# Optimization experiments

Measured on AMD Instinct MI355X. Metric: run time of the kernel, lower is better.

Reference implementation:

```python
import jax, jax.numpy as jnp
import numpy as np

B, D, L = 4096, 128, 4
ALPHA = 1.0
SLOPE = 0.1  # LeakyReLU negative slope


def _leaky(h):
    return jnp.where(h > 0, h, SLOPE * h)


def _dleaky(h):
    return jnp.where(h > 0, 1.0, SLOPE).astype(h.dtype)


def setup_inputs() -> dict:
    key = jax.random.key(0)
    ks = jax.random.split(key, 7)
    scale = 0.5 / np.sqrt(D)  # keep residual roughly Lipschitz < 1
    x = jax.random.normal(ks[0], (B, D), jnp.float32)
    W1 = jax.random.normal(ks[1], (L, D, D), jnp.float32) * scale
    b1 = jax.random.normal(ks[2], (L, D), jnp.float32) * 0.01
    W2 = jax.random.normal(ks[3], (L, D, D), jnp.float32) * scale
    b2 = jax.random.normal(ks[4], (L, D), jnp.float32) * 0.01
    W3 = jax.random.normal(ks[5], (L, D, D), jnp.float32) * scale
    b3 = jax.random.normal(ks[6], (L, D), jnp.float32) * 0.01
    return {"x": x, "W1": W1, "b1": b1, "W2": W2, "b2": b2, "W3": W3, "b3": b3}


def reference(x, W1, b1, W2, b2, W3, b3):
    logdet = jnp.zeros(x.shape[0], x.dtype)
    for i in range(L):  # small fixed number of structurally distinct blocks
        w1, w2, w3 = W1[i], W2[i], W3[i]
        # --- block forward: x <- x + alpha * f(x) ---
        h1 = x @ w1.T + b1[i]
        h2 = _leaky(h1) @ w2.T + b2[i]
        f = _leaky(h2) @ w3.T + b3[i]
        x = x + ALPHA * f
        # --- log|det J_f| evaluated at the NEW x (as in the original code) ---
        g1 = x @ w1.T + b1[i]          # [B, D] pre-activation 1
        d1 = _dleaky(g1)
        g2 = _leaky(g1) @ w2.T + b2[i]  # [B, D] pre-activation 2
        d2 = _dleaky(g2)
        # J[b] = w3 @ diag(d2[b]) @ w2 @ diag(d1[b]) @ w1  -> [B, D, D]
        J = (w3[None, :, :] * d2[:, None, :]) @ w2
        J = (J * d1[:, None, :]) @ w1
        s = jnp.linalg.svd(J, compute_uv=False)  # [B, D] singular values
        logdet = logdet + jnp.sum(jnp.log(s), axis=-1)
    return x, logdet
```

## Files before the change

kernel.cpp:

```cpp
#include <hip/hip_runtime.h>

typedef __attribute__((ext_vector_type(8))) short short8;
typedef __attribute__((ext_vector_type(4))) float float4f;
typedef __attribute__((ext_vector_type(4))) unsigned short us4;

#define PITCH 136
#define ROWS 32
#define LOG_SLOPE -2.302585092994046f
#define LN2 0.6931471805599453f
#define NBLK 140
#define LDS_BYTES 69760
#define WS_BIAS 4160
#define WS_WPLANES 8192
#define NWELEM 196608

__device__ __forceinline__ float bf2f(unsigned int u) {
    return __builtin_bit_cast(float, u << 16);
}
__device__ __forceinline__ unsigned short f2bf(float f) {
    unsigned int x = __builtin_bit_cast(unsigned int, f);
    x += 0x7fff + ((x >> 16) & 1);
    return (unsigned short)(x >> 16);
}
__device__ __forceinline__ float4f vmsub(float4f a, float s, float4f b) {
    a[0] -= s * b[0]; a[1] -= s * b[1]; a[2] -= s * b[2]; a[3] -= s * b[3];
    return a;
}
__device__ __forceinline__ float4f vscale(float4f a, float s) {
    a[0] *= s; a[1] *= s; a[2] *= s; a[3] *= s;
    return a;
}

__device__ __forceinline__ void bar_lgkm() {
    asm volatile("s_waitcnt lgkmcnt(0)\n\ts_barrier" ::: "memory");
}

template<int ISF32>
__device__ __forceinline__ float ldv(const void* p, int i) {
    if (ISF32) return ((const float*)p)[i];
    return bf2f(((const unsigned short*)p)[i]);
}

__device__ __forceinline__ int detect_f32(const unsigned short* W1u, int lane) {
    unsigned int u = W1u[lane * 2];
    unsigned int e = (u >> 7) & 0xFF;
    int bad = (e < 64) || (e > 135);
    return __ballot(bad) != 0ull;
}

__device__ __forceinline__ float4f mfma16(short8 a, short8 b, float4f c) {
    return __builtin_amdgcn_mfma_f32_16x16x32_bf16(a, b, c, 0, 0, 0);
}

__device__ __forceinline__ void split8(float4f a, float4f b, short8& hi, short8& lo) {
#pragma unroll
    for (int j = 0; j < 4; ++j) {
        float v = a[j]; unsigned short h = f2bf(v);
        hi[j] = (short)h; lo[j] = (short)f2bf(v - bf2f(h));
        v = b[j]; h = f2bf(v);
        hi[4 + j] = (short)h; lo[4 + j] = (short)f2bf(v - bf2f(h));
    }
}

__global__ void k_prep(const void* __restrict__ W1, const void* __restrict__ W2,
                       const void* __restrict__ W3, const void* __restrict__ b1,
                       const void* __restrict__ b2, const void* __restrict__ b3,
                       float* __restrict__ ws) {
    const int tid = threadIdx.x, bid = blockIdx.x;
    const int isf32 = detect_f32((const unsigned short*)W1, tid & 63);
    unsigned short* whi = (unsigned short*)(ws + WS_WPLANES);
    unsigned short* wlo = whi + NWELEM;
    if (bid < 96) {
        int s = (bid * 256 + tid) * 8;
        int mat = s >> 14, off = s & 16383;
        int wsel = mat >> 2;
        const void* Wm = wsel == 0 ? W1 : (wsel == 1 ? W2 : W3);
        int src = (mat & 3) * 16384 + off;
        short8 hi, lo;
        if (isf32) {
            const float* p = (const float*)Wm + src;
            split8(*(const float4f*)p, *(const float4f*)(p + 4), hi, lo);
        } else {
            hi = *(const short8*)((const unsigned short*)Wm + src);
            lo = (short8){0, 0, 0, 0, 0, 0, 0, 0};
        }
        int c = off >> 7, k = off & 127;
        int kk = k >> 5, q = (k >> 3) & 3;
        int cb = c >> 4, m = c & 15;
        int noff = kk * 4096 + cb * 512 + m * 32 + q * 8;
        *(short8*)(whi + mat * 16384 + noff) = hi;
        *(short8*)(wlo + mat * 16384 + noff) = lo;
    } else {
        for (int e = tid; e < 1536; e += 256) {
            int bsel = e >> 9, idx = e & 511;
            const void* bp = bsel == 0 ? b1 : (bsel == 1 ? b2 : b3);
            ws[WS_BIAS + e] = isf32 ? ((const float*)bp)[idx]
                                    : bf2f(((const unsigned short*)bp)[idx]);
        }
        if (tid == 0) ((int*)ws)[0] = 0;
    }
}

template<int ISF32> struct WT { short8 v[ISF32 ? 16 : 8]; };

template<int ISF32>
__device__ __forceinline__ WT<ISF32> loadW(const unsigned short* __restrict__ wh,
                                           const unsigned short* __restrict__ wl,
                                           int cb, int mq) {
    WT<ISF32> r;
#pragma unroll
    for (int kk = 0; kk < 4; ++kk) {
        const int o0 = kk * 4096 + cb * 512 + mq;
        const int o1 = o0 + 512;
        if (ISF32) {
            r.v[kk * 4 + 0] = *(const short8*)(wh + o0);
            r.v[kk * 4 + 1] = *(const short8*)(wh + o1);
            r.v[kk * 4 + 2] = *(const short8*)(wl + o0);
            r.v[kk * 4 + 3] = *(const short8*)(wl + o1);
        } else {
            r.v[kk * 2 + 0] = *(const short8*)(wh + o0);
            r.v[kk * 2 + 1] = *(const short8*)(wh + o1);
        }
    }
    return r;
}

template<int MODE, int DOLOAD, int ISF32>
__device__ __forceinline__ WT<ISF32> matvec(const WT<ISF32>& w,
        const unsigned short* inh, const unsigned short* inl,
        unsigned short* outh, unsigned short* outl,
        const unsigned short* resh, const unsigned short* resl,
        const unsigned short* __restrict__ nwh, const unsigned short* __restrict__ nwl,
        const float* __restrict__ bias,
        int lane, int colb, int* cnt) {
    const int m = lane & 15, q = lane >> 4;
    float4f b0 = *(const float4f*)(bias + colb + q * 4);
    float4f b1 = *(const float4f*)(bias + colb + 16 + q * 4);
    float4f acc[2][2];
    acc[0][0] = b0; acc[0][1] = b1;
    acc[1][0] = b0; acc[1][1] = b1;
    bar_lgkm();
    WT<ISF32> wn;
    if constexpr (DOLOAD) {
        wn = loadW<ISF32>(nwh, nwl, colb >> 4, m * 32 + q * 8);
    }
#pragma unroll
    for (int kk = 0; kk < 4; ++kk) {
        const int kc = kk * 32 + q * 8;
#pragma unroll
        for (int rt = 0; rt < 2; ++rt) {
            short8 xh = *(const short8*)(inh + (rt * 16 + m) * PITCH + kc);
            short8 xl = *(const short8*)(inl + (rt * 16 + m) * PITCH + kc);
            if (ISF32) {
                acc[rt][0] = mfma16(w.v[kk * 4 + 0], xh, acc[rt][0]);
                acc[rt][0] = mfma16(w.v[kk * 4 + 0], xl, acc[rt][0]);
                acc[rt][0] = mfma16(w.v[kk * 4 + 2], xh, acc[rt][0]);
                acc[rt][1] = mfma16(w.v[kk * 4 + 1], xh, acc[rt][1]);
                acc[rt][1] = mfma16(w.v[kk * 4 + 1], xl, acc[rt][1]);
                acc[rt][1] = mfma16(w.v[kk * 4 + 3], xh, acc[rt][1]);
            } else {
                acc[rt][0] = mfma16(w.v[kk * 2 + 0], xh, acc[rt][0]);
                acc[rt][0] = mfma16(w.v[kk * 2 + 0], xl, acc[rt][0]);
                acc[rt][1] = mfma16(w.v[kk * 2 + 1], xh, acc[rt][1]);
                acc[rt][1] = mfma16(w.v[kk * 2 + 1], xl, acc[rt][1]);
            }
        }
    }
    int cc[2] = {0, 0};
#pragma unroll
    for (int rt = 0; rt < 2; ++rt) {
#pragma unroll
        for (int ct = 0; ct < 2; ++ct) {
            float4f v = acc[rt][ct];
            const int o = (rt * 16 + m) * PITCH + colb + ct * 16 + q * 4;
            if (MODE == 1) {
                us4 rh = *(const us4*)(resh + o);
                us4 rl = *(const us4*)(resl + o);
#pragma unroll
                for (int j = 0; j < 4; ++j) v[j] += bf2f(rh[j]) + bf2f(rl[j]);
            }
            if (MODE >= 2) {
#pragma unroll
                for (int j = 0; j < 4; ++j) cc[rt] += (v[j] <= 0.0f) ? 1 : 0;
            }
            if (MODE == 0 || MODE == 2) {
#pragma unroll
                for (int j = 0; j < 4; ++j) v[j] = v[j] > 0.0f ? v[j] : 0.1f * v[j];
            }
            if (MODE != 3) {
                us4 h, l;
#pragma unroll
                for (int j = 0; j < 4; ++j) {
                    unsigned short hh = f2bf(v[j]);
                    h[j] = hh;
                    l[j] = f2bf(v[j] - bf2f(hh));
                }
                *(us4*)(outh + o) = h;
                *(us4*)(outl + o) = l;
            }
        }
    }
    if (MODE >= 2) {
#pragma unroll
        for (int rt = 0; rt < 2; ++rt) {
            int c = cc[rt];
            c += __shfl_xor(c, 16);
            c += __shfl_xor(c, 32);
            if (q == 0) atomicAdd(&cnt[rt * 16 + m], c);
        }
    }
    if constexpr (DOLOAD) return wn;
    else return w;
}

template<int ISF32>
__device__ __forceinline__ void fwd(int bid, int tid, int lane, char* ldsb,
                                    const void* x, const float* ws, void* out,
                                    float* wsw) {
    unsigned short* P = (unsigned short*)ldsb;
    unsigned short* Ah = P;
    unsigned short* Al = P + 1 * ROWS * PITCH;
    unsigned short* Bh = P + 2 * ROWS * PITCH;
    unsigned short* Bl = P + 3 * ROWS * PITCH;
    unsigned short* Th = P + 4 * ROWS * PITCH;
    unsigned short* Tl = P + 5 * ROWS * PITCH;
    unsigned short* Uh = P + 6 * ROWS * PITCH;
    unsigned short* Ul = P + 7 * ROWS * PITCH;
    int* cnt = (int*)(P + 8 * ROWS * PITCH);
    const unsigned short* whi = (const unsigned short*)(ws + WS_WPLANES);
    const unsigned short* wlo = whi + NWELEM;
    const float* bias = ws + WS_BIAS;
    const int r0 = bid * ROWS;
    const int m = lane & 15, q = lane >> 4;
    const int colb = (tid >> 6) * 32;
    WT<ISF32> wA = loadW<ISF32>(whi, wlo, colb >> 4, m * 32 + q * 8);
    WT<ISF32> wB, wC;
    for (int e = tid; e < ROWS * 128; e += 256) {
        int r = e >> 7, c = e & 127;
        float v = ldv<ISF32>(x, (r0 + r) * 128 + c);
        unsigned short h = f2bf(v);
        Ah[r * PITCH + c] = h;
        Al[r * PITCH + c] = f2bf(v - bf2f(h));
    }
    if (tid < ROWS) cnt[tid] = 0;
    unsigned short *curh = Ah, *curl = Al, *othh = Bh, *othl = Bl;
#pragma unroll 1
    for (int layer = 0; layer < 4; ++layer) {
        const unsigned short* w2h = whi + (4 + layer) * 16384;
        const unsigned short* w2l = wlo + (4 + layer) * 16384;
        const unsigned short* w3h = whi + (8 + layer) * 16384;
        const unsigned short* w3l = wlo + (8 + layer) * 16384;
        const unsigned short* n1h = whi + ((layer + 1) & 3) * 16384;
        const unsigned short* n1l = wlo + ((layer + 1) & 3) * 16384;
        const float* b1p = bias + layer * 128;
        const float* b2p = bias + 512 + layer * 128;
        const float* b3p = bias + 1024 + layer * 128;
        wB = matvec<0, 1, ISF32>(wA, curh, curl, Th, Tl, 0, 0, w2h, w2l, b1p, lane, colb, cnt);
        wC = matvec<0, 1, ISF32>(wB, Th, Tl, Uh, Ul, 0, 0, w3h, w3l, b2p, lane, colb, cnt);
        matvec<1, 0, ISF32>(wC, Uh, Ul, othh, othl, curh, curl, 0, 0, b3p, lane, colb, cnt);
        matvec<2, 0, ISF32>(wA, othh, othl, Th, Tl, 0, 0, 0, 0, b1p, lane, colb, cnt);
        wA = matvec<3, 1, ISF32>(wB, Th, Tl, Th, Tl, 0, 0, n1h, n1l, b2p, lane, colb, cnt);
        unsigned short* t;
        t = curh; curh = othh; othh = t;
        t = curl; curl = othl; othl = t;
    }
    bar_lgkm();
    for (int e = tid; e < ROWS * 128; e += 256) {
        int r = e >> 7, c = e & 127;
        float v = bf2f(curh[r * PITCH + c]) + bf2f(curl[r * PITCH + c]);
        if (ISF32) ((float*)out)[(r0 + r) * 128 + c] = v;
        else ((unsigned short*)out)[(r0 + r) * 128 + c] = f2bf(v);
    }
    if (tid < ROWS) wsw[64 + r0 + tid] = (float)cnt[tid];
}

template<int ISF32>
__device__ __forceinline__ float lu_logdet(int id, int tid, float* lds,
        const void* W1, const void* W2, const void* W3) {
    const int wsel = id % 3;
    const void* Wm = (wsel == 0 ? W1 : (wsel == 1 ? W2 : W3));
    const int ofs = (id / 3) * 16384;
    const int tx = tid & 31, ty = tid >> 5;
    float* rowbuf = lds;
    float* colbuf = lds + 1024;
    float4f V[16];
#pragma unroll
    for (int m = 0; m < 16; ++m) {
        int base = ofs + (ty + 8 * m) * 128 + 4 * tx;
        if (ISF32) {
            V[m] = *(const float4f*)((const float*)Wm + base);
        } else {
            ushort4 u = *(const ushort4*)((const unsigned short*)Wm + base);
            V[m] = (float4f){bf2f(u.x), bf2f(u.y), bf2f(u.z), bf2f(u.w)};
        }
    }
    if (ty < 4) *(float4f*)&rowbuf[ty * 128 + 4 * tx] = V[0];
    if (tx == 0) {
#pragma unroll
        for (int j = 0; j < 4; ++j) {
#pragma unroll
            for (int mg = 0; mg < 4; ++mg) {
                float4f t = {V[mg * 4 + 0][j], V[mg * 4 + 1][j],
                             V[mg * 4 + 2][j], V[mg * 4 + 3][j]};
                *(float4f*)&colbuf[j * 128 + ty * 16 + mg * 4] = t;
            }
        }
    }
    __syncthreads();
    float logacc = 0.0f;
#pragma unroll 1
    for (int kap = 0; kap < 32; ++kap) {
        const int K = kap * 4;
        const int buf = (kap & 1) * 512;
        float4f D[4], R[4], C[4][4];
#pragma unroll
        for (int j = 0; j < 4; ++j) {
            D[j] = *(const float4f*)&rowbuf[buf + j * 128 + K];
            R[j] = *(const float4f*)&rowbuf[buf + j * 128 + 4 * tx];
#pragma unroll
            for (int mg = 0; mg < 4; ++mg)
                C[j][mg] = *(const float4f*)&colbuf[buf + j * 128 + ty * 16 + mg * 4];
        }
        float p0 = D[0][0], i0 = 1.0f / p0;
        float l10 = D[1][0] * i0, l20 = D[2][0] * i0, l30 = D[3][0] * i0;
        D[1] = vmsub(D[1], l10, D[0]); R[1] = vmsub(R[1], l10, R[0]);
        D[2] = vmsub(D[2], l20, D[0]); R[2] = vmsub(R[2], l20, R[0]);
        D[3] = vmsub(D[3], l30, D[0]); R[3] = vmsub(R[3], l30, R[0]);
        float p1 = D[1][1], i1 = 1.0f / p1;
        float l21 = D[2][1] * i1, l31 = D[3][1] * i1;
        D[2] = vmsub(D[2], l21, D[1]); R[2] = vmsub(R[2], l21, R[1]);
        D[3] = vmsub(D[3], l31, D[1]); R[3] = vmsub(R[3], l31, R[1]);
        float p2 = D[2][2], i2 = 1.0f / p2;
        float l32 = D[3][2] * i2;
        D[3] = vmsub(D[3], l32, D[2]); R[3] = vmsub(R[3], l32, R[2]);
        float p3 = D[3][3], i3 = 1.0f / p3;
        logacc += __log2f(fabsf(p0)) + __log2f(fabsf(p1))
                + __log2f(fabsf(p2)) + __log2f(fabsf(p3));
        float4f X3 = vscale(R[3], i3);
        float4f X2 = vscale(vmsub(R[2], D[2][3], X3), i2);
        float4f X1 = vscale(vmsub(vmsub(R[1], D[1][2], X2), D[1][3], X3), i1);
        float4f X0 = vscale(vmsub(vmsub(vmsub(R[0], D[0][1], X1),
                                        D[0][2], X2), D[0][3], X3), i0);
#pragma unroll
        for (int mg = 0; mg < 4; ++mg) {
#pragma unroll
            for (int e = 0; e < 4; ++e) {
                float4f v = V[mg * 4 + e];
                v = vmsub(v, C[0][mg][e], X0);
                v = vmsub(v, C[1][mg][e], X1);
                v = vmsub(v, C[2][mg][e], X2);
                v = vmsub(v, C[3][mg][e], X3);
                V[mg * 4 + e] = v;
            }
        }
        if (kap < 31) {
            const int nbuf = ((kap + 1) & 1) * 512;
            const int tb = (kap & 1) ? 0 : 4;
            const int mn = (kap + 1) >> 1;
            if (ty >= tb && ty < tb + 4) {
                float4f val;
                switch (mn) {
                case 0:  val = V[0];  break; case 1:  val = V[1];  break;
                case 2:  val = V[2];  break; case 3:  val = V[3];  break;
                case 4:  val = V[4];  break; case 5:  val = V[5];  break;
                case 6:  val = V[6];  break; case 7:  val = V[7];  break;
                case 8:  val = V[8];  break; case 9:  val = V[9];  break;
                case 10: val = V[10]; break; case 11: val = V[11]; break;
                case 12: val = V[12]; break; case 13: val = V[13]; break;
                case 14: val = V[14]; break; default: val = V[15]; break;
                }
                *(float4f*)&rowbuf[nbuf + (ty - tb) * 128 + 4 * tx] = val;
            }
            if (tx == kap + 1) {
#pragma unroll
                for (int j = 0; j < 4; ++j) {
#pragma unroll
                    for (int mg = 0; mg < 4; ++mg) {
                        float4f t = {V[mg * 4 + 0][j], V[mg * 4 + 1][j],
                                     V[mg * 4 + 2][j], V[mg * 4 + 3][j]};
                        *(float4f*)&colbuf[nbuf + j * 128 + ty * 16 + mg * 4] = t;
                    }
                }
            }
        }
        __syncthreads();
    }
    return logacc * LN2;
}

__global__ __launch_bounds__(256, 1) void k_main(
        const void* __restrict__ x,
        const void* __restrict__ W1, const void* __restrict__ b1,
        const void* __restrict__ W2, const void* __restrict__ b2,
        const void* __restrict__ W3, const void* __restrict__ b3,
        void* __restrict__ out, float* __restrict__ ws) {
    extern __shared__ __align__(16) char ldsb[];
    __shared__ int s_last;
    const int tid = threadIdx.x;
    const int lane = tid & 63;
    const int isf32 = detect_f32((const unsigned short*)W1, lane);

    if (blockIdx.x < 12) {
        float ld = isf32 ? lu_logdet<1>(blockIdx.x, tid, (float*)ldsb, W1, W2, W3)
                         : lu_logdet<0>(blockIdx.x, tid, (float*)ldsb, W1, W2, W3);
        if (tid == 0) ws[2 + blockIdx.x] = ld;
    } else {
        const int bid = blockIdx.x - 12;
        if (isf32) fwd<1>(bid, tid, lane, ldsb, x, ws, out, ws);
        else       fwd<0>(bid, tid, lane, ldsb, x, ws, out, ws);
    }

    __threadfence();
    if (tid == 0) s_last = (atomicAdd((int*)ws, 1) == NBLK - 1);
    __syncthreads();
    if (!s_last) return;
    __threadfence();
    float s = 0.0f;
#pragma unroll
    for (int i = 0; i < 12; ++i) s += ws[2 + i];
    for (int b = tid; b < 4096; b += 256) {
        float v = s + LOG_SLOPE * ws[64 + b];
        if (isf32) ((float*)out)[524288 + b] = v;
        else ((unsigned short*)out)[524288 + b] = f2bf(v);
    }
}

extern "C" void kernel_launch(void* const* d_in, const int* in_sizes, int n_in,
                              void* d_out, int out_size, void* d_ws, size_t ws_size,
                              hipStream_t stream) {
    const void* x  = d_in[0];
    const void* W1 = d_in[1];
    const void* b1 = d_in[2];
    const void* W2 = d_in[3];
    const void* b2 = d_in[4];
    const void* W3 = d_in[5];
    const void* b3 = d_in[6];
    float* ws = (float*)d_ws;

    hipLaunchKernelGGL(k_prep, dim3(97), dim3(256), 0, stream,
                       W1, W2, W3, b1, b2, b3, ws);
    hipLaunchKernelGGL(k_main, dim3(NBLK), dim3(256), LDS_BYTES, stream,
                       x, W1, b1, W2, b2, W3, b3, d_out, ws);
}
```

Measured before the change: 119.4 us.

## Interleave two LU factorizations per block to share barriers and cut block count

Each LU-logdet block now factors two weight matrices at once, interleaving their elimination steps inside one loop so the two sets of independent work overlap and share one barrier per step. The block count falls from 12 LU blocks to 6, so the grid shrinks from 140 to 134. The intent is to hide the per-step LDS and barrier latency of the serial LU chain with independent work. The cost is doubled register state per thread (two sets of 16 float4 values), which risks spills, and twice the work per LU block on the critical path.

```diff
diff --git a/kernel.cpp b/kernel.cpp
--- a/kernel.cpp
+++ b/kernel.cpp
@@ -8,7 +8,7 @@
 #define ROWS 32
 #define LOG_SLOPE -2.302585092994046f
 #define LN2 0.6931471805599453f
-#define NBLK 140
+#define NBLK 134
 #define LDS_BYTES 69760
 #define WS_BIAS 4160
 #define WS_WPLANES 8192
@@ -275,117 +275,120 @@
 }
 
 template<int ISF32>
-__device__ __forceinline__ float lu_logdet(int id, int tid, float* lds,
-        const void* W1, const void* W2, const void* W3) {
+struct LUState { float4f V[16]; };
+
+template<int ISF32>
+__device__ __forceinline__ void lu_init(LUState<ISF32>& S, int id,
+        const void* W1, const void* W2, const void* W3, int tx, int ty) {
     const int wsel = id % 3;
     const void* Wm = (wsel == 0 ? W1 : (wsel == 1 ? W2 : W3));
     const int ofs = (id / 3) * 16384;
-    const int tx = tid & 31, ty = tid >> 5;
-    float* rowbuf = lds;
-    float* colbuf = lds + 1024;
-    float4f V[16];
 #pragma unroll
     for (int m = 0; m < 16; ++m) {
         int base = ofs + (ty + 8 * m) * 128 + 4 * tx;
         if (ISF32) {
-            V[m] = *(const float4f*)((const float*)Wm + base);
+            S.V[m] = *(const float4f*)((const float*)Wm + base);
         } else {
             ushort4 u = *(const ushort4*)((const unsigned short*)Wm + base);
-            V[m] = (float4f){bf2f(u.x), bf2f(u.y), bf2f(u.z), bf2f(u.w)};
-        }
-    }
-    if (ty < 4) *(float4f*)&rowbuf[ty * 128 + 4 * tx] = V[0];
+            S.V[m] = (float4f){bf2f(u.x), bf2f(u.y), bf2f(u.z), bf2f(u.w)};
+        }
+    }
+}
+
+template<int ISF32>
+__device__ __forceinline__ void lu_stage0(LUState<ISF32>& S,
+        float* rowbuf, float* colbuf, int tx, int ty) {
+    if (ty < 4) *(float4f*)&rowbuf[ty * 128 + 4 * tx] = S.V[0];
     if (tx == 0) {
 #pragma unroll
         for (int j = 0; j < 4; ++j) {
 #pragma unroll
             for (int mg = 0; mg < 4; ++mg) {
-                float4f t = {V[mg * 4 + 0][j], V[mg * 4 + 1][j],
-                             V[mg * 4 + 2][j], V[mg * 4 + 3][j]};
+                float4f t = {S.V[mg * 4 + 0][j], S.V[mg * 4 + 1][j],
+                             S.V[mg * 4 + 2][j], S.V[mg * 4 + 3][j]};
                 *(float4f*)&colbuf[j * 128 + ty * 16 + mg * 4] = t;
             }
         }
     }
-    __syncthreads();
-    float logacc = 0.0f;
-#pragma unroll 1
-    for (int kap = 0; kap < 32; ++kap) {
-        const int K = kap * 4;
-        const int buf = (kap & 1) * 512;
-        float4f D[4], R[4], C[4][4];
-#pragma unroll
-        for (int j = 0; j < 4; ++j) {
-            D[j] = *(const float4f*)&rowbuf[buf + j * 128 + K];
-            R[j] = *(const float4f*)&rowbuf[buf + j * 128 + 4 * tx];
-#pragma unroll
-            for (int mg = 0; mg < 4; ++mg)
-                C[j][mg] = *(const float4f*)&colbuf[buf + j * 128 + ty * 16 + mg * 4];
-        }
-        float p0 = D[0][0], i0 = 1.0f / p0;
-        float l10 = D[1][0] * i0, l20 = D[2][0] * i0, l30 = D[3][0] * i0;
-        D[1] = vmsub(D[1], l10, D[0]); R[1] = vmsub(R[1], l10, R[0]);
-        D[2] = vmsub(D[2], l20, D[0]); R[2] = vmsub(R[2], l20, R[0]);
-        D[3] = vmsub(D[3], l30, D[0]); R[3] = vmsub(R[3], l30, R[0]);
-        float p1 = D[1][1], i1 = 1.0f / p1;
-        float l21 = D[2][1] * i1, l31 = D[3][1] * i1;
-        D[2] = vmsub(D[2], l21, D[1]); R[2] = vmsub(R[2], l21, R[1]);
-        D[3] = vmsub(D[3], l31, D[1]); R[3] = vmsub(R[3], l31, R[1]);
-        float p2 = D[2][2], i2 = 1.0f / p2;
-        float l32 = D[3][2] * i2;
-        D[3] = vmsub(D[3], l32, D[2]); R[3] = vmsub(R[3], l32, R[2]);
-        float p3 = D[3][3], i3 = 1.0f / p3;
-        logacc += __log2f(fabsf(p0)) + __log2f(fabsf(p1))
-                + __log2f(fabsf(p2)) + __log2f(fabsf(p3));
-        float4f X3 = vscale(R[3], i3);
-        float4f X2 = vscale(vmsub(R[2], D[2][3], X3), i2);
-        float4f X1 = vscale(vmsub(vmsub(R[1], D[1][2], X2), D[1][3], X3), i1);
-        float4f X0 = vscale(vmsub(vmsub(vmsub(R[0], D[0][1], X1),
-                                        D[0][2], X2), D[0][3], X3), i0);
-#pragma unroll
-        for (int mg = 0; mg < 4; ++mg) {
-#pragma unroll
-            for (int e = 0; e < 4; ++e) {
-                float4f v = V[mg * 4 + e];
-                v = vmsub(v, C[0][mg][e], X0);
-                v = vmsub(v, C[1][mg][e], X1);
-                v = vmsub(v, C[2][mg][e], X2);
-                v = vmsub(v, C[3][mg][e], X3);
-                V[mg * 4 + e] = v;
-            }
-        }
-        if (kap < 31) {
-            const int nbuf = ((kap + 1) & 1) * 512;
-            const int tb = (kap & 1) ? 0 : 4;
-            const int mn = (kap + 1) >> 1;
-            if (ty >= tb && ty < tb + 4) {
-                float4f val;
-                switch (mn) {
-                case 0:  val = V[0];  break; case 1:  val = V[1];  break;
-                case 2:  val = V[2];  break; case 3:  val = V[3];  break;
-                case 4:  val = V[4];  break; case 5:  val = V[5];  break;
-                case 6:  val = V[6];  break; case 7:  val = V[7];  break;
-                case 8:  val = V[8];  break; case 9:  val = V[9];  break;
-                case 10: val = V[10]; break; case 11: val = V[11]; break;
-                case 12: val = V[12]; break; case 13: val = V[13]; break;
-                case 14: val = V[14]; break; default: val = V[15]; break;
+}
+
+template<int ISF32>
+__device__ __forceinline__ float lu_step(LUState<ISF32>& S,
+        float* rowbuf, float* colbuf, int kap, int tx, int ty) {
+    const int K = kap * 4;
+    const int buf = (kap & 1) * 512;
+    float4f D[4], R[4], C[4][4];
+#pragma unroll
+    for (int j = 0; j < 4; ++j) {
+        D[j] = *(const float4f*)&rowbuf[buf + j * 128 + K];
+        R[j] = *(const float4f*)&rowbuf[buf + j * 128 + 4 * tx];
+#pragma unroll
+        for (int mg = 0; mg < 4; ++mg)
+            C[j][mg] = *(const float4f*)&colbuf[buf + j * 128 + ty * 16 + mg * 4];
+    }
+    float p0 = D[0][0], i0 = 1.0f / p0;
+    float l10 = D[1][0] * i0, l20 = D[2][0] * i0, l30 = D[3][0] * i0;
+    D[1] = vmsub(D[1], l10, D[0]); R[1] = vmsub(R[1], l10, R[0]);
+    D[2] = vmsub(D[2], l20, D[0]); R[2] = vmsub(R[2], l20, R[0]);
+    D[3] = vmsub(D[3], l30, D[0]); R[3] = vmsub(R[3], l30, R[0]);
+    float p1 = D[1][1], i1 = 1.0f / p1;
+    float l21 = D[2][1] * i1, l31 = D[3][1] * i1;
+    D[2] = vmsub(D[2], l21, D[1]); R[2] = vmsub(R[2], l21, R[1]);
+    D[3] = vmsub(D[3], l31, D[1]); R[3] = vmsub(R[3], l31, R[1]);
+    float p2 = D[2][2], i2 = 1.0f / p2;
+    float l32 = D[3][2] * i2;
+    D[3] = vmsub(D[3], l32, D[2]); R[3] = vmsub(R[3], l32, R[2]);
+    float p3 = D[3][3], i3 = 1.0f / p3;
+    float lg = __log2f(fabsf(p0)) + __log2f(fabsf(p1))
+             + __log2f(fabsf(p2)) + __log2f(fabsf(p3));
+    float4f X3 = vscale(R[3], i3);
+    float4f X2 = vscale(vmsub(R[2], D[2][3], X3), i2);
+    float4f X1 = vscale(vmsub(vmsub(R[1], D[1][2], X2), D[1][3], X3), i1);
+    float4f X0 = vscale(vmsub(vmsub(vmsub(R[0], D[0][1], X1),
+                                    D[0][2], X2), D[0][3], X3), i0);
+#pragma unroll
+    for (int mg = 0; mg < 4; ++mg) {
+#pragma unroll
+        for (int e = 0; e < 4; ++e) {
+            float4f v = S.V[mg * 4 + e];
+            v = vmsub(v, C[0][mg][e], X0);
+            v = vmsub(v, C[1][mg][e], X1);
+            v = vmsub(v, C[2][mg][e], X2);
+            v = vmsub(v, C[3][mg][e], X3);
+            S.V[mg * 4 + e] = v;
+        }
+    }
+    if (kap < 31) {
+        const int nbuf = ((kap + 1) & 1) * 512;
+        const int tb = (kap & 1) ? 0 : 4;
+        const int mn = (kap + 1) >> 1;
+        if (ty >= tb && ty < tb + 4) {
+            float4f val;
+            switch (mn) {
+            case 0:  val = S.V[0];  break; case 1:  val = S.V[1];  break;
+            case 2:  val = S.V[2];  break; case 3:  val = S.V[3];  break;
+            case 4:  val = S.V[4];  break; case 5:  val = S.V[5];  break;
+            case 6:  val = S.V[6];  break; case 7:  val = S.V[7];  break;
+            case 8:  val = S.V[8];  break; case 9:  val = S.V[9];  break;
+            case 10: val = S.V[10]; break; case 11: val = S.V[11]; break;
+            case 12: val = S.V[12]; break; case 13: val = S.V[13]; break;
+            case 14: val = S.V[14]; break; default: val = S.V[15]; break;
+            }
+            *(float4f*)&rowbuf[nbuf + (ty - tb) * 128 + 4 * tx] = val;
+        }
+        if (tx == kap + 1) {
+#pragma unroll
+            for (int j = 0; j < 4; ++j) {
+#pragma unroll
+                for (int mg = 0; mg < 4; ++mg) {
+                    float4f t = {S.V[mg * 4 + 0][j], S.V[mg * 4 + 1][j],
+                                 S.V[mg * 4 + 2][j], S.V[mg * 4 + 3][j]};
+                    *(float4f*)&colbuf[nbuf + j * 128 + ty * 16 + mg * 4] = t;
                 }
-                *(float4f*)&rowbuf[nbuf + (ty - tb) * 128 + 4 * tx] = val;
-            }
-            if (tx == kap + 1) {
-#pragma unroll
-                for (int j = 0; j < 4; ++j) {
-#pragma unroll
-                    for (int mg = 0; mg < 4; ++mg) {
-                        float4f t = {V[mg * 4 + 0][j], V[mg * 4 + 1][j],
-                                     V[mg * 4 + 2][j], V[mg * 4 + 3][j]};
-                        *(float4f*)&colbuf[nbuf + j * 128 + ty * 16 + mg * 4] = t;
-                    }
-                }
-            }
-        }
-        __syncthreads();
-    }
-    return logacc * LN2;
+            }
+        }
+    }
+    return lg;
 }
 
 __global__ __launch_bounds__(256, 1) void k_main(
@@ -400,12 +403,46 @@
     const int lane = tid & 63;
     const int isf32 = detect_f32((const unsigned short*)W1, lane);
 
-    if (blockIdx.x < 12) {
-        float ld = isf32 ? lu_logdet<1>(blockIdx.x, tid, (float*)ldsb, W1, W2, W3)
-                         : lu_logdet<0>(blockIdx.x, tid, (float*)ldsb, W1, W2, W3);
-        if (tid == 0) ws[2 + blockIdx.x] = ld;
+    if (blockIdx.x < 6) {
+        const int tx = tid & 31, ty = tid >> 5;
+        float* lds = (float*)ldsb;
+        float* rbA = lds;          float* cbA = lds + 1024;
+        float* rbB = lds + 2048;   float* cbB = lds + 3072;
+        const int idA = blockIdx.x * 2, idB = idA + 1;
+        float la = 0.0f, lb = 0.0f;
+        if (isf32) {
+            LUState<1> SA, SB;
+            lu_init<1>(SA, idA, W1, W2, W3, tx, ty);
+            lu_init<1>(SB, idB, W1, W2, W3, tx, ty);
+            lu_stage0<1>(SA, rbA, cbA, tx, ty);
+            lu_stage0<1>(SB, rbB, cbB, tx, ty);
+            __syncthreads();
+#pragma unroll 1
+            for (int kap = 0; kap < 32; ++kap) {
+                la += lu_step<1>(SA, rbA, cbA, kap, tx, ty);
+                lb += lu_step<1>(SB, rbB, cbB, kap, tx, ty);
+                __syncthreads();
+            }
+        } else {
+            LUState<0> SA, SB;
+            lu_init<0>(SA, idA, W1, W2, W3, tx, ty);
+            lu_init<0>(SB, idB, W1, W2, W3, tx, ty);
+            lu_stage0<0>(SA, rbA, cbA, tx, ty);
+            lu_stage0<0>(SB, rbB, cbB, tx, ty);
+            __syncthreads();
+#pragma unroll 1
+            for (int kap = 0; kap < 32; ++kap) {
+                la += lu_step<0>(SA, rbA, cbA, kap, tx, ty);
+                lb += lu_step<0>(SB, rbB, cbB, kap, tx, ty);
+                __syncthreads();
+            }
+        }
+        if (tid == 0) {
+            ws[2 + idA] = la * LN2;
+            ws[2 + idB] = lb * LN2;
+        }
     } else {
-        const int bid = blockIdx.x - 12;
+        const int bid = blockIdx.x - 6;
         if (isf32) fwd<1>(bid, tid, lane, ldsb, x, ws, out, ws);
         else       fwd<0>(bid, tid, lane, ldsb, x, ws, out, ws);
     }
```

New measurement: 181.0 us. +51.5%, slower.

## Widen LU panel from 4 to 8 columns to halve barrier-separated steps

Applied to the files above, without the earlier changes.

The blocked LU used for the log-determinant now eliminates 8 pivot columns per step instead of 4. That halves the number of outer iterations and their __syncthreads barriers, and each thread's trailing update does more FMAs per LDS round. The row and column panel buffers double in size, and column-panel writes are split across two lanes. In exchange there is more register pressure (8-wide D, R, X and C arrays) and a longer serial 8x8 factorisation inside each step.

```diff
diff --git a/kernel.cpp b/kernel.cpp
--- a/kernel.cpp
+++ b/kernel.cpp
@@ -282,7 +282,7 @@
     const int ofs = (id / 3) * 16384;
     const int tx = tid & 31, ty = tid >> 5;
     float* rowbuf = lds;
-    float* colbuf = lds + 1024;
+    float* colbuf = lds + 2048;
     float4f V[16];
 #pragma unroll
     for (int m = 0; m < 16; ++m) {
@@ -294,91 +294,96 @@
             V[m] = (float4f){bf2f(u.x), bf2f(u.y), bf2f(u.z), bf2f(u.w)};
         }
     }
-    if (ty < 4) *(float4f*)&rowbuf[ty * 128 + 4 * tx] = V[0];
-    if (tx == 0) {
+    *(float4f*)&rowbuf[ty * 128 + 4 * tx] = V[0];
+    if (tx < 2) {
 #pragma unroll
         for (int j = 0; j < 4; ++j) {
 #pragma unroll
             for (int mg = 0; mg < 4; ++mg) {
                 float4f t = {V[mg * 4 + 0][j], V[mg * 4 + 1][j],
                              V[mg * 4 + 2][j], V[mg * 4 + 3][j]};
-                *(float4f*)&colbuf[j * 128 + ty * 16 + mg * 4] = t;
+                *(float4f*)&colbuf[(tx * 4 + j) * 128 + ty * 16 + mg * 4] = t;
             }
         }
     }
     __syncthreads();
     float logacc = 0.0f;
 #pragma unroll 1
-    for (int kap = 0; kap < 32; ++kap) {
-        const int K = kap * 4;
-        const int buf = (kap & 1) * 512;
-        float4f D[4], R[4], C[4][4];
-#pragma unroll
-        for (int j = 0; j < 4; ++j) {
-            D[j] = *(const float4f*)&rowbuf[buf + j * 128 + K];
-            R[j] = *(const float4f*)&rowbuf[buf + j * 128 + 4 * tx];
-#pragma unroll
-            for (int mg = 0; mg < 4; ++mg)
-                C[j][mg] = *(const float4f*)&colbuf[buf + j * 128 + ty * 16 + mg * 4];
-        }
-        float p0 = D[0][0], i0 = 1.0f / p0;
-        float l10 = D[1][0] * i0, l20 = D[2][0] * i0, l30 = D[3][0] * i0;
-        D[1] = vmsub(D[1], l10, D[0]); R[1] = vmsub(R[1], l10, R[0]);
-        D[2] = vmsub(D[2], l20, D[0]); R[2] = vmsub(R[2], l20, R[0]);
-        D[3] = vmsub(D[3], l30, D[0]); R[3] = vmsub(R[3], l30, R[0]);
-        float p1 = D[1][1], i1 = 1.0f / p1;
-        float l21 = D[2][1] * i1, l31 = D[3][1] * i1;
-        D[2] = vmsub(D[2], l21, D[1]); R[2] = vmsub(R[2], l21, R[1]);
-        D[3] = vmsub(D[3], l31, D[1]); R[3] = vmsub(R[3], l31, R[1]);
-        float p2 = D[2][2], i2 = 1.0f / p2;
-        float l32 = D[3][2] * i2;
-        D[3] = vmsub(D[3], l32, D[2]); R[3] = vmsub(R[3], l32, R[2]);
-        float p3 = D[3][3], i3 = 1.0f / p3;
-        logacc += __log2f(fabsf(p0)) + __log2f(fabsf(p1))
-                + __log2f(fabsf(p2)) + __log2f(fabsf(p3));
-        float4f X3 = vscale(R[3], i3);
-        float4f X2 = vscale(vmsub(R[2], D[2][3], X3), i2);
-        float4f X1 = vscale(vmsub(vmsub(R[1], D[1][2], X2), D[1][3], X3), i1);
-        float4f X0 = vscale(vmsub(vmsub(vmsub(R[0], D[0][1], X1),
-                                        D[0][2], X2), D[0][3], X3), i0);
+    for (int kap = 0; kap < 16; ++kap) {
+        const int K = kap * 8;
+        const int buf = (kap & 1) * 1024;
+        float4f Da[8], Db[8], R[8];
+#pragma unroll
+        for (int j = 0; j < 8; ++j) {
+            Da[j] = *(const float4f*)&rowbuf[buf + j * 128 + K];
+            Db[j] = *(const float4f*)&rowbuf[buf + j * 128 + K + 4];
+            R[j]  = *(const float4f*)&rowbuf[buf + j * 128 + 4 * tx];
+        }
+        float ivv[8];
+#pragma unroll
+        for (int i = 0; i < 8; ++i) {
+            float p = (i < 4) ? Da[i][i] : Db[i][i - 4];
+            float inv = 1.0f / p;
+            ivv[i] = inv;
+            logacc += __log2f(fabsf(p));
+#pragma unroll
+            for (int j = i + 1; j < 8; ++j) {
+                float l = ((i < 4) ? Da[j][i] : Db[j][i - 4]) * inv;
+                Da[j] = vmsub(Da[j], l, Da[i]);
+                Db[j] = vmsub(Db[j], l, Db[i]);
+                R[j]  = vmsub(R[j],  l, R[i]);
+            }
+        }
+        float4f X[8];
+#pragma unroll
+        for (int j = 7; j >= 0; --j) {
+            float4f t = R[j];
+#pragma unroll
+            for (int k = j + 1; k < 8; ++k) {
+                float u = (k < 4) ? Da[j][k] : Db[j][k - 4];
+                t = vmsub(t, u, X[k]);
+            }
+            X[j] = vscale(t, ivv[j]);
+        }
 #pragma unroll
         for (int mg = 0; mg < 4; ++mg) {
+            float4f C[8];
+#pragma unroll
+            for (int jj = 0; jj < 8; ++jj)
+                C[jj] = *(const float4f*)&colbuf[buf + jj * 128 + ty * 16 + mg * 4];
 #pragma unroll
             for (int e = 0; e < 4; ++e) {
                 float4f v = V[mg * 4 + e];
-                v = vmsub(v, C[0][mg][e], X0);
-                v = vmsub(v, C[1][mg][e], X1);
-                v = vmsub(v, C[2][mg][e], X2);
-                v = vmsub(v, C[3][mg][e], X3);
+#pragma unroll
+                for (int jj = 0; jj < 8; ++jj)
+                    v = vmsub(v, C[jj][e], X[jj]);
                 V[mg * 4 + e] = v;
             }
         }
-        if (kap < 31) {
-            const int nbuf = ((kap + 1) & 1) * 512;
-            const int tb = (kap & 1) ? 0 : 4;
-            const int mn = (kap + 1) >> 1;
-            if (ty >= tb && ty < tb + 4) {
-                float4f val;
-                switch (mn) {
-                case 0:  val = V[0];  break; case 1:  val = V[1];  break;
-                case 2:  val = V[2];  break; case 3:  val = V[3];  break;
-                case 4:  val = V[4];  break; case 5:  val = V[5];  break;
-                case 6:  val = V[6];  break; case 7:  val = V[7];  break;
-                case 8:  val = V[8];  break; case 9:  val = V[9];  break;
-                case 10: val = V[10]; break; case 11: val = V[11]; break;
-                case 12: val = V[12]; break; case 13: val = V[13]; break;
-                case 14: val = V[14]; break; default: val = V[15]; break;
-                }
-                *(float4f*)&rowbuf[nbuf + (ty - tb) * 128 + 4 * tx] = val;
-            }
-            if (tx == kap + 1) {
+        if (kap < 15) {
+            const int nbuf = ((kap + 1) & 1) * 1024;
+            const int mn = kap + 1;
+            float4f val;
+            switch (mn) {
+            case 1:  val = V[1];  break; case 2:  val = V[2];  break;
+            case 3:  val = V[3];  break; case 4:  val = V[4];  break;
+            case 5:  val = V[5];  break; case 6:  val = V[6];  break;
+            case 7:  val = V[7];  break; case 8:  val = V[8];  break;
+            case 9:  val = V[9];  break; case 10: val = V[10]; break;
+            case 11: val = V[11]; break; case 12: val = V[12]; break;
+            case 13: val = V[13]; break; case 14: val = V[14]; break;
+            default: val = V[15]; break;
+            }
+            *(float4f*)&rowbuf[nbuf + ty * 128 + 4 * tx] = val;
+            if ((tx >> 1) == mn) {
+                const int half = (tx & 1) * 4;
 #pragma unroll
                 for (int j = 0; j < 4; ++j) {
 #pragma unroll
                     for (int mg = 0; mg < 4; ++mg) {
                         float4f t = {V[mg * 4 + 0][j], V[mg * 4 + 1][j],
                                      V[mg * 4 + 2][j], V[mg * 4 + 3][j]};
-                        *(float4f*)&colbuf[nbuf + j * 128 + ty * 16 + mg * 4] = t;
+                        *(float4f*)&colbuf[nbuf + (half + j) * 128 + ty * 16 + mg * 4] = t;
                     }
                 }
             }
```

Measured after the change: 120.1 us. No clear change (+0.5%).

## Fold weight-prep kernel into main kernel with a grid-wide spin barrier

Applied to the files above, without the earlier changes.

Removes the separate k_prep launch and has the 128 forward blocks split and relayout the weights into the workspace themselves, then wait on an atomic counter until every block has finished before loading weights. A memset replaces the prep kernel's counter reset. This removes one kernel launch and its inter-kernel gap, and overlaps the x load with the prep. In exchange it relies on all 128 forward blocks being co-resident; if they are not, the spin-wait can deadlock.

```diff
diff --git a/kernel.cpp b/kernel.cpp
--- a/kernel.cpp
+++ b/kernel.cpp
@@ -59,45 +59,6 @@
         hi[j] = (short)h; lo[j] = (short)f2bf(v - bf2f(h));
         v = b[j]; h = f2bf(v);
         hi[4 + j] = (short)h; lo[4 + j] = (short)f2bf(v - bf2f(h));
-    }
-}
-
-__global__ void k_prep(const void* __restrict__ W1, const void* __restrict__ W2,
-                       const void* __restrict__ W3, const void* __restrict__ b1,
-                       const void* __restrict__ b2, const void* __restrict__ b3,
-                       float* __restrict__ ws) {
-    const int tid = threadIdx.x, bid = blockIdx.x;
-    const int isf32 = detect_f32((const unsigned short*)W1, tid & 63);
-    unsigned short* whi = (unsigned short*)(ws + WS_WPLANES);
-    unsigned short* wlo = whi + NWELEM;
-    if (bid < 96) {
-        int s = (bid * 256 + tid) * 8;
-        int mat = s >> 14, off = s & 16383;
-        int wsel = mat >> 2;
-        const void* Wm = wsel == 0 ? W1 : (wsel == 1 ? W2 : W3);
-        int src = (mat & 3) * 16384 + off;
-        short8 hi, lo;
-        if (isf32) {
-            const float* p = (const float*)Wm + src;
-            split8(*(const float4f*)p, *(const float4f*)(p + 4), hi, lo);
-        } else {
-            hi = *(const short8*)((const unsigned short*)Wm + src);
-            lo = (short8){0, 0, 0, 0, 0, 0, 0, 0};
-        }
-        int c = off >> 7, k = off & 127;
-        int kk = k >> 5, q = (k >> 3) & 3;
-        int cb = c >> 4, m = c & 15;
-        int noff = kk * 4096 + cb * 512 + m * 32 + q * 8;
-        *(short8*)(whi + mat * 16384 + noff) = hi;
-        *(short8*)(wlo + mat * 16384 + noff) = lo;
-    } else {
-        for (int e = tid; e < 1536; e += 256) {
-            int bsel = e >> 9, idx = e & 511;
-            const void* bp = bsel == 0 ? b1 : (bsel == 1 ? b2 : b3);
-            ws[WS_BIAS + e] = isf32 ? ((const float*)bp)[idx]
-                                    : bf2f(((const unsigned short*)bp)[idx]);
-        }
-        if (tid == 0) ((int*)ws)[0] = 0;
     }
 }
 
@@ -215,8 +176,14 @@
 
 template<int ISF32>
 __device__ __forceinline__ void fwd(int bid, int tid, int lane, char* ldsb,
-                                    const void* x, const float* ws, void* out,
-                                    float* wsw) {
+                                    const void* x,
+                                    const void* __restrict__ W1,
+                                    const void* __restrict__ W2,
+                                    const void* __restrict__ W3,
+                                    const void* __restrict__ b1,
+                                    const void* __restrict__ b2,
+                                    const void* __restrict__ b3,
+                                    float* ws, void* out) {
     unsigned short* P = (unsigned short*)ldsb;
     unsigned short* Ah = P;
     unsigned short* Al = P + 1 * ROWS * PITCH;
@@ -227,14 +194,48 @@
     unsigned short* Uh = P + 6 * ROWS * PITCH;
     unsigned short* Ul = P + 7 * ROWS * PITCH;
     int* cnt = (int*)(P + 8 * ROWS * PITCH);
-    const unsigned short* whi = (const unsigned short*)(ws + WS_WPLANES);
-    const unsigned short* wlo = whi + NWELEM;
+    unsigned short* whi = (unsigned short*)(ws + WS_WPLANES);
+    unsigned short* wlo = whi + NWELEM;
     const float* bias = ws + WS_BIAS;
     const int r0 = bid * ROWS;
     const int m = lane & 15, q = lane >> 4;
     const int colb = (tid >> 6) * 32;
-    WT<ISF32> wA = loadW<ISF32>(whi, wlo, colb >> 4, m * 32 + q * 8);
-    WT<ISF32> wB, wC;
+
+    {
+        int idx = bid * 256 + tid;
+        if (idx < 24576) {
+            int s = idx * 8;
+            int mat = s >> 14, off = s & 16383;
+            int wsel = mat >> 2;
+            const void* Wm = wsel == 0 ? W1 : (wsel == 1 ? W2 : W3);
+            int src = (mat & 3) * 16384 + off;
+            short8 hi, lo;
+            if (ISF32) {
+                const float* p = (const float*)Wm + src;
+                split8(*(const float4f*)p, *(const float4f*)(p + 4), hi, lo);
+            } else {
+                hi = *(const short8*)((const unsigned short*)Wm + src);
+                lo = (short8){0, 0, 0, 0, 0, 0, 0, 0};
+            }
+            int c = off >> 7, k = off & 127;
+            int noff = (k >> 5) * 4096 + (c >> 4) * 512 + (c & 15) * 32
+                     + ((k >> 3) & 3) * 8;
+            *(short8*)(whi + mat * 16384 + noff) = hi;
+            *(short8*)(wlo + mat * 16384 + noff) = lo;
+        }
+        if (bid == 96) {
+            for (int e = tid; e < 1536; e += 256) {
+                int bsel = e >> 9, bidx = e & 511;
+                const void* bp = bsel == 0 ? b1 : (bsel == 1 ? b2 : b3);
+                ws[WS_BIAS + e] = ISF32 ? ((const float*)bp)[bidx]
+                                        : bf2f(((const unsigned short*)bp)[bidx]);
+            }
+        }
+        __threadfence();
+        __syncthreads();
+        if (tid == 0) atomicAdd((int*)ws + 1, 1);
+    }
+
     for (int e = tid; e < ROWS * 128; e += 256) {
         int r = e >> 7, c = e & 127;
         float v = ldv<ISF32>(x, (r0 + r) * 128 + c);
@@ -243,6 +244,15 @@
         Al[r * PITCH + c] = f2bf(v - bf2f(h));
     }
     if (tid < ROWS) cnt[tid] = 0;
+
+    if (tid == 0) {
+        while (atomicAdd((int*)ws + 1, 0) < 128) {}
+    }
+    __syncthreads();
+    __threadfence();
+
+    WT<ISF32> wA = loadW<ISF32>(whi, wlo, colb >> 4, m * 32 + q * 8);
+    WT<ISF32> wB, wC;
     unsigned short *curh = Ah, *curl = Al, *othh = Bh, *othl = Bl;
 #pragma unroll 1
     for (int layer = 0; layer < 4; ++layer) {
@@ -271,7 +281,7 @@
         if (ISF32) ((float*)out)[(r0 + r) * 128 + c] = v;
         else ((unsigned short*)out)[(r0 + r) * 128 + c] = f2bf(v);
     }
-    if (tid < ROWS) wsw[64 + r0 + tid] = (float)cnt[tid];
+    if (tid < ROWS) ws[64 + r0 + tid] = (float)cnt[tid];
 }
 
 template<int ISF32>
@@ -406,8 +416,8 @@
         if (tid == 0) ws[2 + blockIdx.x] = ld;
     } else {
         const int bid = blockIdx.x - 12;
-        if (isf32) fwd<1>(bid, tid, lane, ldsb, x, ws, out, ws);
-        else       fwd<0>(bid, tid, lane, ldsb, x, ws, out, ws);
+        if (isf32) fwd<1>(bid, tid, lane, ldsb, x, W1, W2, W3, b1, b2, b3, ws, out);
+        else       fwd<0>(bid, tid, lane, ldsb, x, W1, W2, W3, b1, b2, b3, ws, out);
     }
 
     __threadfence();
@@ -437,8 +447,7 @@
     const void* b3 = d_in[6];
     float* ws = (float*)d_ws;
 
-    hipLaunchKernelGGL(k_prep, dim3(97), dim3(256), 0, stream,
-                       W1, W2, W3, b1, b2, b3, ws);
+    hipMemsetAsync(ws, 0, 8, stream);
     hipLaunchKernelGGL(k_main, dim3(NBLK), dim3(256), LDS_BYTES, stream,
                        x, W1, b1, W2, b2, W3, b3, d_out, ws);
 }
```

Result: slower. 132.4 us (+10.8%).
